# Kernel optimization log

Measured on AMD Instinct MI355X. Metric: run time of the kernel, lower is better.

Reference implementation:

```python
import jax, jax.numpy as jnp
import numpy as np

N_NODES = 100000
N_EDGES = 3200000
NFEAT, H1, H2, NCLASS = 512, 300, 200, 40


def setup_inputs() -> dict:
    key = jax.random.key(0)
    ks = jax.random.split(key, 8)
    x = jax.random.normal(ks[0], (N_NODES, NFEAT), dtype=jnp.float32)
    edge_index = jax.random.randint(ks[1], (2, N_EDGES), 0, N_NODES, dtype=jnp.int32)
    edge_weight = jax.random.uniform(ks[2], (N_EDGES,), dtype=jnp.float32)
    def glorot(k, fi, fo):
        s = 1.0 / np.sqrt(fi)
        return jax.random.uniform(k, (fi, fo), jnp.float32, -s, s)
    w1 = glorot(ks[3], NFEAT, H1)
    w2 = glorot(ks[4], H1, H2)
    w3 = glorot(ks[5], H2, NCLASS)
    return {
        'x': x, 'edge_index': edge_index, 'edge_weight': edge_weight,
        'w1': w1, 'b1': jnp.zeros((H1,), jnp.float32),
        'w2': w2, 'b2': jnp.zeros((H2,), jnp.float32),
        'w3': w3, 'b3': jnp.zeros((NCLASS,), jnp.float32),
    }


def _gcn_layer(h, edge_index, edge_weight, w, b):
    # support = h @ W ; out = A @ support + b  (A given as weighted edge list)
    support = h @ w                                   # [N, out]
    src, dst = edge_index[0], edge_index[1]
    msgs = support[src] * edge_weight[:, None]        # gather + scale, [E, out]
    agg = jax.ops.segment_sum(msgs, dst, num_segments=h.shape[0])
    return agg + b


def reference(x, edge_index, edge_weight, w1, b1, w2, b2, w3, b3):
    h1 = jax.nn.relu(_gcn_layer(x, edge_index, edge_weight, w1, b1))
    h2 = jax.nn.relu(_gcn_layer(h1, edge_index, edge_weight, w2, b2))
    logits = _gcn_layer(h2, edge_index, edge_weight, w3, b3)
    return jax.nn.softmax(logits, axis=1)
```

## Files before the change

### kernel.cpp

```cpp
#include <hip/hip_runtime.h>
#include <hip/hip_bf16.h>
#include <hip/hip_fp16.h>
#include <math.h>

#define NFEAT 512
#define H1 300
#define H2 200
#define NCLASS 40

typedef __attribute__((ext_vector_type(8))) _Float16 half8;
typedef __attribute__((ext_vector_type(4))) float f32x4;
typedef __attribute__((ext_vector_type(2))) unsigned int u32x2;

__device__ __forceinline__ void stage16(const void* gptr, void* ldsptr) {
    __builtin_amdgcn_global_load_lds(
        (const __attribute__((address_space(1))) unsigned int*)gptr,
        (__attribute__((address_space(3))) unsigned int*)ldsptr,
        16, 0, 0);
}

__device__ __forceinline__ unsigned short f2h(float f) {
    return __half_as_ushort(__float2half(f));
}
__device__ __forceinline__ float h2f(unsigned short u) {
    return __half2float(__ushort_as_half(u));
}
__device__ __forceinline__ float2 h2f2(unsigned int u) {
    __half2 h = *reinterpret_cast<__half2*>(&u);
    return __half22float2(h);
}
__device__ __forceinline__ unsigned pack2h(float a, float b) {
    return (unsigned)f2h(a) | ((unsigned)f2h(b) << 16);
}


__global__ __launch_bounds__(256) void count_dst_kernel(const int* __restrict__ dst,
                                                        int* __restrict__ counts, int E) {
    int i = blockIdx.x * blockDim.x + threadIdx.x;
    if (i < E) atomicAdd(&counts[dst[i]], 1);
}

__global__ __launch_bounds__(1024) void scan_kernel(const int* __restrict__ counts,
                                                    int* __restrict__ row_ptr,
                                                    int* __restrict__ nextp, int N) {
    __shared__ int sums[1024];
    const int tid = threadIdx.x;
    const int CH = (N + 1023) >> 10;
    const int b = tid * CH;
    const int e = min(b + CH, N);
    int s = 0;
    for (int i = b; i < e; i++) s += counts[i];
    sums[tid] = s;
    __syncthreads();
    #pragma unroll
    for (int off = 1; off < 1024; off <<= 1) {
        int t = (tid >= off) ? sums[tid - off] : 0;
        __syncthreads();
        sums[tid] += t;
        __syncthreads();
    }
    int run = (tid > 0) ? sums[tid - 1] : 0;
    for (int i = b; i < e; i++) {
        row_ptr[i] = run;
        nextp[i] = run;
        run += counts[i];
    }
    if (tid == 0) row_ptr[N] = sums[1023];
}

__global__ __launch_bounds__(256) void fill_csr_kernel(const int* __restrict__ src,
                                                       const int* __restrict__ dst,
                                                       const float* __restrict__ ew,
                                                       int* __restrict__ next,
                                                       int2* __restrict__ csr_sw, int E) {
    int i = blockIdx.x * blockDim.x + threadIdx.x;
    if (i < E) {
        int d = dst[i];
        int pos = atomicAdd(&next[d], 1);
        csr_sw[pos] = make_int2(src[i], __float_as_int(ew[i]));
    }
}


__global__ __launch_bounds__(256) void convert_x_kernel(const float* __restrict__ x,
                                                        unsigned short* __restrict__ X16,
                                                        int total8) {
    int stride = gridDim.x * 256;
    for (int i = blockIdx.x * 256 + threadIdx.x; i < total8; i += stride) {
        const float* p = x + (size_t)i * 8;
        float4 a = *(const float4*)p;
        float4 b = *(const float4*)(p + 4);
        half8 h;
        h[0] = (_Float16)a.x; h[1] = (_Float16)a.y;
        h[2] = (_Float16)a.z; h[3] = (_Float16)a.w;
        h[4] = (_Float16)b.x; h[5] = (_Float16)b.y;
        h[6] = (_Float16)b.z; h[7] = (_Float16)b.w;
        *(half8*)(X16 + (size_t)i * 8) = h;
    }
}


__global__ __launch_bounds__(256) void split_weights_kernel(
        const float* __restrict__ w1, const float* __restrict__ w2, const float* __restrict__ w3,
        unsigned short* __restrict__ W1H, unsigned short* __restrict__ W1L,
        unsigned short* __restrict__ W2H, unsigned short* __restrict__ W2L,
        unsigned short* __restrict__ W3H, unsigned short* __restrict__ W3L) {
    int i = blockIdx.x * 256 + threadIdx.x;
    const float* w; unsigned short *H, *L; int K, N, KP;
    if (i < 163840) {
        w = w1; H = W1H; L = W1L; K = 512; N = 300; KP = 512;
    } else if (i < 163840 + 81920) {
        i -= 163840; w = w2; H = W2H; L = W2L; K = 300; N = 200; KP = 320;
    } else {
        i -= 245760; w = w3; H = W3H; L = W3L; K = 200; N = 40; KP = 256;
    }
    int n = i / KP, k = i - n * KP;
    float a = (n < N && k < K) ? w[(size_t)k * N + n] : 0.f;
    unsigned short h = f2h(a);
    H[i] = h;
    L[i] = f2h(a - h2f(h));
}


template <int KPAD, int NT, bool AF32>
__global__ __launch_bounds__(256, 3) void gemm_f16_kernel(
        const void* __restrict__ A_,
        const unsigned short* __restrict__ Bhi, const unsigned short* __restrict__ Blo,
        unsigned short* __restrict__ C, int M, int NP, int MT) {
    __shared__ short Bs_hi[4096];
    __shared__ short Bs_lo[4096];

    const int id = blockIdx.x;
    const int g  = id / (8 * NT);
    const int r  = id % (8 * NT);
    const int nt = r >> 3;
    const int x  = r & 7;
    const int mt = g * 8 + x;
    if (mt >= MT) return;

    const int tid = threadIdx.x;
    const int wave = tid >> 6, lane = tid & 63;
    const int lm = lane & 15, quad = lane >> 4;
    const int bm = mt * 256, bn = nt * 64;

    f32x4 acc[4][4] = {};

    for (int k0 = 0; k0 < KPAD; k0 += 64) {
        #pragma unroll
        for (int i = 0; i < 2; i++) {
            int t = i * 256 + tid;
            int n = t >> 3;
            int c = (t & 7) ^ (n & 7);
            size_t goff = (size_t)(bn + n) * KPAD + (size_t)(k0 + c * 8);
            int lbase = (i * 256 + wave * 64) * 8;
            stage16(Bhi + goff, Bs_hi + lbase);
            stage16(Blo + goff, Bs_lo + lbase);
        }
        __syncthreads();

        #pragma unroll
        for (int h = 0; h < 2; h++) {
            const int cidx = h * 4 + quad;
            half8 a[4], bh[4], bl[4];
            #pragma unroll
            for (int i = 0; i < 4; i++) {
                int row = bm + wave * 64 + i * 16 + lm;
                row = row < M ? row : M - 1;
                size_t off = (size_t)row * KPAD + (size_t)(k0 + cidx * 8);
                if (AF32) {
                    const float* ap = (const float*)A_ + off;
                    float4 p = *(const float4*)ap;
                    float4 q = *(const float4*)(ap + 4);
                    half8 t8;
                    t8[0] = (_Float16)p.x; t8[1] = (_Float16)p.y;
                    t8[2] = (_Float16)p.z; t8[3] = (_Float16)p.w;
                    t8[4] = (_Float16)q.x; t8[5] = (_Float16)q.y;
                    t8[6] = (_Float16)q.z; t8[7] = (_Float16)q.w;
                    a[i] = t8;
                } else {
                    a[i] = *(const half8*)((const unsigned short*)A_ + off);
                }
            }
            #pragma unroll
            for (int j = 0; j < 4; j++) {
                int n = j * 16 + lm;
                int off = (n * 8 + (cidx ^ (n & 7))) * 8;
                bh[j] = *(const half8*)(Bs_hi + off);
                bl[j] = *(const half8*)(Bs_lo + off);
            }
            #pragma unroll
            for (int i = 0; i < 4; i++)
                #pragma unroll
                for (int j = 0; j < 4; j++) {
                    acc[i][j] = __builtin_amdgcn_mfma_f32_16x16x32_f16(a[i], bh[j], acc[i][j], 0, 0, 0);
                    acc[i][j] = __builtin_amdgcn_mfma_f32_16x16x32_f16(a[i], bl[j], acc[i][j], 0, 0, 0);
                }
        }
        __syncthreads();
    }

    #pragma unroll
    for (int i = 0; i < 4; i++) {
        #pragma unroll
        for (int j = 0; j < 4; j++) {
            #pragma unroll
            for (int r2 = 0; r2 < 4; r2++) {
                int row = bm + wave * 64 + i * 16 + quad * 4 + r2;
                int col = bn + j * 16 + lm;
                if (row < M)
                    C[(size_t)row * NP + col] = f2h(acc[i][j][r2]);
            }
        }
    }
}


template <int F, int NP>
__global__ __launch_bounds__(256) void spmm_relu_f16_kernel(
        const int* __restrict__ row_ptr, const int2* __restrict__ csr_sw,
        const unsigned short* __restrict__ support, const float* __restrict__ bias,
        unsigned short* __restrict__ outp, int N) {
    constexpr int F4 = F / 4;
    constexpr int NP4 = NP / 4;
    constexpr int NCH = (F4 + 63) / 64;
    constexpr int NCHW = (NP4 + 63) / 64;

    int row = blockIdx.x * 4 + (threadIdx.x >> 6);
    int lane = threadIdx.x & 63;
    if (row >= N) return;
    int beg = row_ptr[row], end = row_ptr[row + 1];

    float acc[NCHW][4] = {};

    int e = beg;
    int nb8 = (end - beg) >> 3;
    if (nb8 > 0) {
        int2 swbuf[8];
        #pragma unroll
        for (int q = 0; q < 8; q++) swbuf[q] = csr_sw[e + q];
        for (int b = 0; b < nb8; b++) {
            int s_[8]; float w_[8];
            #pragma unroll
            for (int q = 0; q < 8; q++) {
                s_[q] = __builtin_amdgcn_readfirstlane(swbuf[q].x);
                w_[q] = __uint_as_float((unsigned)__builtin_amdgcn_readfirstlane(swbuf[q].y));
            }
            u32x2 u[8][NCH];
            #pragma unroll
            for (int q = 0; q < 8; q++) {
                const unsigned short* sp = support + (size_t)s_[q] * NP;
                #pragma unroll
                for (int j = 0; j < NCH; j++) {
                    int f4 = j * 64 + lane;
                    if (f4 < F4) u[q][j] = *(const u32x2*)(sp + f4 * 4);
                }
            }
            int enext = e + 8;
            if (b + 1 < nb8) {
                #pragma unroll
                for (int q = 0; q < 8; q++) swbuf[q] = csr_sw[enext + q];
            }
            #pragma unroll
            for (int q = 0; q < 8; q++) {
                #pragma unroll
                for (int j = 0; j < NCH; j++) {
                    int f4 = j * 64 + lane;
                    if (f4 < F4) {
                        float2 a0 = h2f2(u[q][j].x), a1 = h2f2(u[q][j].y);
                        acc[j][0] += w_[q] * a0.x;
                        acc[j][1] += w_[q] * a0.y;
                        acc[j][2] += w_[q] * a1.x;
                        acc[j][3] += w_[q] * a1.y;
                    }
                }
            }
            e = enext;
        }
    }
    for (; e + 3 < end; e += 4) {
        int s_[4]; float w_[4];
        #pragma unroll
        for (int q = 0; q < 4; q++) {
            int2 sw = csr_sw[e + q];
            s_[q] = __builtin_amdgcn_readfirstlane(sw.x);
            w_[q] = __uint_as_float((unsigned)__builtin_amdgcn_readfirstlane(sw.y));
        }
        u32x2 u[4][NCH];
        #pragma unroll
        for (int q = 0; q < 4; q++) {
            const unsigned short* sp = support + (size_t)s_[q] * NP;
            #pragma unroll
            for (int j = 0; j < NCH; j++) {
                int f4 = j * 64 + lane;
                if (f4 < F4) u[q][j] = *(const u32x2*)(sp + f4 * 4);
            }
        }
        #pragma unroll
        for (int q = 0; q < 4; q++) {
            #pragma unroll
            for (int j = 0; j < NCH; j++) {
                int f4 = j * 64 + lane;
                if (f4 < F4) {
                    float2 a0 = h2f2(u[q][j].x), a1 = h2f2(u[q][j].y);
                    acc[j][0] += w_[q] * a0.x;
                    acc[j][1] += w_[q] * a0.y;
                    acc[j][2] += w_[q] * a1.x;
                    acc[j][3] += w_[q] * a1.y;
                }
            }
        }
    }
    for (; e < end; e++) {
        int2 sw = csr_sw[e];
        int ssrc = __builtin_amdgcn_readfirstlane(sw.x);
        float w0 = __uint_as_float((unsigned)__builtin_amdgcn_readfirstlane(sw.y));
        const unsigned short* sp = support + (size_t)ssrc * NP;
        #pragma unroll
        for (int j = 0; j < NCH; j++) {
            int f4 = j * 64 + lane;
            if (f4 < F4) {
                u32x2 u = *(const u32x2*)(sp + f4 * 4);
                float2 a0 = h2f2(u.x), a1 = h2f2(u.y);
                acc[j][0] += w0 * a0.x;
                acc[j][1] += w0 * a0.y;
                acc[j][2] += w0 * a1.x;
                acc[j][3] += w0 * a1.y;
            }
        }
    }

    #pragma unroll
    for (int j = 0; j < NCHW; j++) {
        int f4 = j * 64 + lane;
        if (f4 < NP4) {
            bool real = f4 < F4;
            float4 bb = real ? ((const float4*)bias)[f4] : make_float4(0, 0, 0, 0);
            float v0 = real ? fmaxf(acc[j][0] + bb.x, 0.f) : 0.f;
            float v1 = real ? fmaxf(acc[j][1] + bb.y, 0.f) : 0.f;
            float v2 = real ? fmaxf(acc[j][2] + bb.z, 0.f) : 0.f;
            float v3 = real ? fmaxf(acc[j][3] + bb.w, 0.f) : 0.f;
            u32x2 w;
            w.x = pack2h(v0, v1);
            w.y = pack2h(v2, v3);
            *(u32x2*)(outp + (size_t)row * NP + f4 * 4) = w;
        }
    }
}


__global__ __launch_bounds__(256) void spmm_softmax_kernel(
        const int* __restrict__ row_ptr, const int2* __restrict__ csr_sw,
        const unsigned short* __restrict__ support, const float* __restrict__ bias,
        float* __restrict__ out, int N) {
    int row = blockIdx.x * 4 + (threadIdx.x >> 6);
    int lane = threadIdx.x & 63;
    if (row >= N) return;
    int beg = row_ptr[row], end = row_ptr[row + 1];

    const int g = lane / 20;
    const int t = lane - g * 20;
    const bool lact = lane < 60;

    float a0 = 0.f, a1 = 0.f;
    for (int e = beg; e < end; e += 3) {
        int ei = e + g;
        bool v = lact && (ei < end);
        int2 sw = csr_sw[v ? ei : beg];
        float w = v ? __int_as_float(sw.y) : 0.f;
        unsigned u = *(const unsigned*)(support + (size_t)sw.x * 64 + t * 2);
        float2 aa = h2f2(u);
        a0 += w * aa.x;
        a1 += w * aa.y;
    }
    a0 += __shfl(a0, lane + 20) + __shfl(a0, lane + 40);
    a1 += __shfl(a1, lane + 20) + __shfl(a1, lane + 40);

    const bool act = lane < 20;
    float v0 = 0.f, v1 = 0.f, m = -INFINITY;
    if (act) {
        float2 bb = ((const float2*)bias)[t];
        v0 = a0 + bb.x;
        v1 = a1 + bb.y;
        m = fmaxf(v0, v1);
    }
    #pragma unroll
    for (int off = 16; off; off >>= 1) m = fmaxf(m, __shfl_xor(m, off));
    float e0 = 0.f, e1 = 0.f;
    if (act) { e0 = expf(v0 - m); e1 = expf(v1 - m); }
    float s = e0 + e1;
    #pragma unroll
    for (int off = 16; off; off >>= 1) s += __shfl_xor(s, off);
    if (act) {
        float inv = 1.f / s;
        *(float2*)(out + (size_t)row * NCLASS + t * 2) = make_float2(e0 * inv, e1 * inv);
    }
}


extern "C" void kernel_launch(void* const* d_in, const int* in_sizes, int n_in,
                              void* d_out, int out_size, void* d_ws, size_t ws_size,
                              hipStream_t stream) {
    const float* x   = (const float*)d_in[0];
    const int*   ei  = (const int*)d_in[1];
    const float* ew  = (const float*)d_in[2];
    const float* w1  = (const float*)d_in[3];
    const float* b1  = (const float*)d_in[4];
    const float* w2  = (const float*)d_in[5];
    const float* b2  = (const float*)d_in[6];
    const float* w3  = (const float*)d_in[7];
    const float* b3  = (const float*)d_in[8];
    float* out = (float*)d_out;

    const int N = in_sizes[0] / NFEAT;
    const int E = in_sizes[2];
    const int* src = ei;
    const int* dst = ei + E;

    const int KP1 = 512, NP1 = 320, NT1 = 5;
    const int KP2 = 320, NP2 = 256, NT2 = 4;
    const int KP3 = 256, NP3 = 64,  NT3 = 1;

    char* base = (char*)d_ws;
    unsigned short* X16 = (unsigned short*)(base);
    unsigned short* H1H = (unsigned short*)(base);
    unsigned short* H2H = (unsigned short*)(base);

    unsigned short* support = (unsigned short*)(base + 102400256);

    size_t wo = 102400256 + 64000256;
    auto walloc = [&](size_t bytes) { void* r = base + wo; wo += (bytes + 255) & ~(size_t)255; return r; };
    unsigned short* W1H = (unsigned short*)walloc((size_t)NP1 * KP1 * 2);
    unsigned short* W1L = (unsigned short*)walloc((size_t)NP1 * KP1 * 2);
    unsigned short* W2H = (unsigned short*)walloc((size_t)NP2 * KP2 * 2);
    unsigned short* W2L = (unsigned short*)walloc((size_t)NP2 * KP2 * 2);
    unsigned short* W3H = (unsigned short*)walloc((size_t)NP3 * KP3 * 2);
    unsigned short* W3L = (unsigned short*)walloc((size_t)NP3 * KP3 * 2);
    int*  counts  = (int*)walloc((size_t)N * 4);
    int*  row_ptr = (int*)walloc((size_t)(N + 1) * 4);
    int*  nextp   = (int*)walloc((size_t)N * 4);
    int2* csr_sw  = (int2*)walloc((size_t)E * 8);

    const int MT = (N + 255) / 256;
    const int G  = (MT + 7) / 8;
    const int wgs = (N + 3) / 4;

    hipMemsetAsync(counts, 0, (size_t)N * 4, stream);
    count_dst_kernel<<<(E + 255) / 256, 256, 0, stream>>>(dst, counts, E);
    scan_kernel<<<1, 1024, 0, stream>>>(counts, row_ptr, nextp, N);
    fill_csr_kernel<<<(E + 255) / 256, 256, 0, stream>>>(src, dst, ew, nextp, csr_sw, E);

    split_weights_kernel<<<1024, 256, 0, stream>>>(w1, w2, w3, W1H, W1L, W2H, W2L, W3H, W3L);
    convert_x_kernel<<<2048, 256, 0, stream>>>(x, X16, N * NFEAT / 8);

    gemm_f16_kernel<KP1, NT1, false><<<G * 8 * NT1, 256, 0, stream>>>(
        X16, W1H, W1L, support, N, NP1, MT);
    spmm_relu_f16_kernel<H1, NP1><<<wgs, 256, 0, stream>>>(row_ptr, csr_sw, support, b1, H1H, N);

    gemm_f16_kernel<KP2, NT2, false><<<G * 8 * NT2, 256, 0, stream>>>(
        H1H, W2H, W2L, support, N, NP2, MT);
    spmm_relu_f16_kernel<H2, NP2><<<wgs, 256, 0, stream>>>(row_ptr, csr_sw, support, b2, H2H, N);

    gemm_f16_kernel<KP3, NT3, false><<<G * 8 * NT3, 256, 0, stream>>>(
        H2H, W3H, W3L, support, N, NP3, MT);
    spmm_softmax_kernel<<<wgs, 256, 0, stream>>>(row_ptr, csr_sw, support, b3, out, N);
}
```

Before: 1.687 ms.

## Restructure SpMM kernels as persistent grid-stride waves with wide per-lane loads

The SpMM kernels become persistent: a fixed grid of 2048 blocks walks rows in grid-stride fashion instead of launching one wave per row. For H1, each lane now loads 8 halfs per neighbor in a single 16-byte load instead of two 8-byte chunks. Edge metadata is fetched with one vector load across lanes and broadcast with readlane, replacing the per-edge scalar loads and separate remainder loops. This cuts launch and instruction overhead, but a fixed grid can leave work unbalanced and partial batches still issue dummy loads with zero weight.

```diff
diff --git a/kernel.cpp b/kernel.cpp
--- a/kernel.cpp
+++ b/kernel.cpp
@@ -216,133 +216,86 @@
 
 
 template <int F, int NP>
-__global__ __launch_bounds__(256) void spmm_relu_f16_kernel(
+__global__ __launch_bounds__(256, 8) void spmm_relu_f16_kernel(
         const int* __restrict__ row_ptr, const int2* __restrict__ csr_sw,
         const unsigned short* __restrict__ support, const float* __restrict__ bias,
         unsigned short* __restrict__ outp, int N) {
-    constexpr int F4 = F / 4;
-    constexpr int NP4 = NP / 4;
-    constexpr int NCH = (F4 + 63) / 64;
-    constexpr int NCHW = (NP4 + 63) / 64;
-
-    int row = blockIdx.x * 4 + (threadIdx.x >> 6);
-    int lane = threadIdx.x & 63;
-    if (row >= N) return;
-    int beg = row_ptr[row], end = row_ptr[row + 1];
-
-    float acc[NCHW][4] = {};
-
-    int e = beg;
-    int nb8 = (end - beg) >> 3;
-    if (nb8 > 0) {
-        int2 swbuf[8];
-        #pragma unroll
-        for (int q = 0; q < 8; q++) swbuf[q] = csr_sw[e + q];
-        for (int b = 0; b < nb8; b++) {
+    constexpr bool WIDE = ((F + 3) / 4 > 64);
+    constexpr int LPE = WIDE ? (F + 7) / 8 : (F + 3) / 4;
+    constexpr int AK  = WIDE ? 8 : 4;
+
+    const int lane = threadIdx.x & 63;
+    const int nwaves = gridDim.x * 4;
+    const int lc = min(lane, LPE - 1);
+
+    for (int row = blockIdx.x * 4 + (threadIdx.x >> 6); row < N; row += nwaves) {
+        const int beg = row_ptr[row], end = row_ptr[row + 1];
+        float acc[AK];
+        #pragma unroll
+        for (int k = 0; k < AK; k++) acc[k] = 0.f;
+
+        int e = beg;
+        int2 swv;
+        if (e < end) swv = csr_sw[e + min(lane, min(end - e, 8) - 1)];
+        while (e < end) {
+            const int m = min(end - e, 8);
+            const int2 cur = swv;
             int s_[8]; float w_[8];
             #pragma unroll
             for (int q = 0; q < 8; q++) {
-                s_[q] = __builtin_amdgcn_readfirstlane(swbuf[q].x);
-                w_[q] = __uint_as_float((unsigned)__builtin_amdgcn_readfirstlane(swbuf[q].y));
-            }
-            u32x2 u[8][NCH];
+                int qq = min(q, m - 1);
+                s_[q] = __builtin_amdgcn_readlane(cur.x, qq);
+                float wv = __uint_as_float((unsigned)__builtin_amdgcn_readlane(cur.y, qq));
+                w_[q] = (q < m) ? wv : 0.f;
+            }
+            half8 u8[8]; u32x2 u4[8];
             #pragma unroll
             for (int q = 0; q < 8; q++) {
                 const unsigned short* sp = support + (size_t)s_[q] * NP;
+                if (WIDE) u8[q] = *(const half8*)(sp + lc * 8);
+                else      u4[q] = *(const u32x2*)(sp + lc * 4);
+            }
+            const int enext = e + m;
+            if (enext < end) swv = csr_sw[enext + min(lane, min(end - enext, 8) - 1)];
+            #pragma unroll
+            for (int q = 0; q < 8; q++) {
+                if (WIDE) {
+                    #pragma unroll
+                    for (int k = 0; k < 8; k++) acc[k] += w_[q] * (float)u8[q][k];
+                } else {
+                    float2 a0 = h2f2(u4[q].x), a1 = h2f2(u4[q].y);
+                    acc[0] += w_[q] * a0.x;
+                    acc[1] += w_[q] * a0.y;
+                    acc[2] += w_[q] * a1.x;
+                    acc[3] += w_[q] * a1.y;
+                }
+            }
+            e = enext;
+        }
+
+        if (WIDE) {
+            if (lane * 8 < NP) {
+                half8 o;
                 #pragma unroll
-                for (int j = 0; j < NCH; j++) {
-                    int f4 = j * 64 + lane;
-                    if (f4 < F4) u[q][j] = *(const u32x2*)(sp + f4 * 4);
+                for (int k = 0; k < 8; k++) {
+                    int f = lane * 8 + k;
+                    float v = 0.f;
+                    if (f < F && lane < LPE) v = fmaxf(acc[k] + bias[f], 0.f);
+                    o[k] = (_Float16)v;
                 }
-            }
-            int enext = e + 8;
-            if (b + 1 < nb8) {
-                #pragma unroll
-                for (int q = 0; q < 8; q++) swbuf[q] = csr_sw[enext + q];
-            }
-            #pragma unroll
-            for (int q = 0; q < 8; q++) {
-                #pragma unroll
-                for (int j = 0; j < NCH; j++) {
-                    int f4 = j * 64 + lane;
-                    if (f4 < F4) {
-                        float2 a0 = h2f2(u[q][j].x), a1 = h2f2(u[q][j].y);
-                        acc[j][0] += w_[q] * a0.x;
-                        acc[j][1] += w_[q] * a0.y;
-                        acc[j][2] += w_[q] * a1.x;
-                        acc[j][3] += w_[q] * a1.y;
-                    }
-                }
-            }
-            e = enext;
-        }
-    }
-    for (; e + 3 < end; e += 4) {
-        int s_[4]; float w_[4];
-        #pragma unroll
-        for (int q = 0; q < 4; q++) {
-            int2 sw = csr_sw[e + q];
-            s_[q] = __builtin_amdgcn_readfirstlane(sw.x);
-            w_[q] = __uint_as_float((unsigned)__builtin_amdgcn_readfirstlane(sw.y));
-        }
-        u32x2 u[4][NCH];
-        #pragma unroll
-        for (int q = 0; q < 4; q++) {
-            const unsigned short* sp = support + (size_t)s_[q] * NP;
-            #pragma unroll
-            for (int j = 0; j < NCH; j++) {
-                int f4 = j * 64 + lane;
-                if (f4 < F4) u[q][j] = *(const u32x2*)(sp + f4 * 4);
-            }
-        }
-        #pragma unroll
-        for (int q = 0; q < 4; q++) {
-            #pragma unroll
-            for (int j = 0; j < NCH; j++) {
-                int f4 = j * 64 + lane;
-                if (f4 < F4) {
-                    float2 a0 = h2f2(u[q][j].x), a1 = h2f2(u[q][j].y);
-                    acc[j][0] += w_[q] * a0.x;
-                    acc[j][1] += w_[q] * a0.y;
-                    acc[j][2] += w_[q] * a1.x;
-                    acc[j][3] += w_[q] * a1.y;
-                }
-            }
-        }
-    }
-    for (; e < end; e++) {
-        int2 sw = csr_sw[e];
-        int ssrc = __builtin_amdgcn_readfirstlane(sw.x);
-        float w0 = __uint_as_float((unsigned)__builtin_amdgcn_readfirstlane(sw.y));
-        const unsigned short* sp = support + (size_t)ssrc * NP;
-        #pragma unroll
-        for (int j = 0; j < NCH; j++) {
-            int f4 = j * 64 + lane;
-            if (f4 < F4) {
-                u32x2 u = *(const u32x2*)(sp + f4 * 4);
-                float2 a0 = h2f2(u.x), a1 = h2f2(u.y);
-                acc[j][0] += w0 * a0.x;
-                acc[j][1] += w0 * a0.y;
-                acc[j][2] += w0 * a1.x;
-                acc[j][3] += w0 * a1.y;
-            }
-        }
-    }
-
-    #pragma unroll
-    for (int j = 0; j < NCHW; j++) {
-        int f4 = j * 64 + lane;
-        if (f4 < NP4) {
-            bool real = f4 < F4;
-            float4 bb = real ? ((const float4*)bias)[f4] : make_float4(0, 0, 0, 0);
-            float v0 = real ? fmaxf(acc[j][0] + bb.x, 0.f) : 0.f;
-            float v1 = real ? fmaxf(acc[j][1] + bb.y, 0.f) : 0.f;
-            float v2 = real ? fmaxf(acc[j][2] + bb.z, 0.f) : 0.f;
-            float v3 = real ? fmaxf(acc[j][3] + bb.w, 0.f) : 0.f;
+                *(half8*)(outp + (size_t)row * NP + lane * 8) = o;
+            }
+        } else {
+            bool real = lane < LPE;
+            float4 bb = real ? ((const float4*)bias)[lane] : make_float4(0, 0, 0, 0);
+            float v0 = real ? fmaxf(acc[0] + bb.x, 0.f) : 0.f;
+            float v1 = real ? fmaxf(acc[1] + bb.y, 0.f) : 0.f;
+            float v2 = real ? fmaxf(acc[2] + bb.z, 0.f) : 0.f;
+            float v3 = real ? fmaxf(acc[3] + bb.w, 0.f) : 0.f;
             u32x2 w;
             w.x = pack2h(v0, v1);
             w.y = pack2h(v2, v3);
-            *(u32x2*)(outp + (size_t)row * NP + f4 * 4) = w;
+            *(u32x2*)(outp + (size_t)row * NP + lane * 4) = w;
         }
     }
 }
@@ -352,47 +305,49 @@
         const int* __restrict__ row_ptr, const int2* __restrict__ csr_sw,
         const unsigned short* __restrict__ support, const float* __restrict__ bias,
         float* __restrict__ out, int N) {
-    int row = blockIdx.x * 4 + (threadIdx.x >> 6);
-    int lane = threadIdx.x & 63;
-    if (row >= N) return;
-    int beg = row_ptr[row], end = row_ptr[row + 1];
+    const int lane = threadIdx.x & 63;
+    const int nwaves = gridDim.x * 4;
 
     const int g = lane / 20;
     const int t = lane - g * 20;
     const bool lact = lane < 60;
 
-    float a0 = 0.f, a1 = 0.f;
-    for (int e = beg; e < end; e += 3) {
-        int ei = e + g;
-        bool v = lact && (ei < end);
-        int2 sw = csr_sw[v ? ei : beg];
-        float w = v ? __int_as_float(sw.y) : 0.f;
-        unsigned u = *(const unsigned*)(support + (size_t)sw.x * 64 + t * 2);
-        float2 aa = h2f2(u);
-        a0 += w * aa.x;
-        a1 += w * aa.y;
-    }
-    a0 += __shfl(a0, lane + 20) + __shfl(a0, lane + 40);
-    a1 += __shfl(a1, lane + 20) + __shfl(a1, lane + 40);
-
-    const bool act = lane < 20;
-    float v0 = 0.f, v1 = 0.f, m = -INFINITY;
-    if (act) {
-        float2 bb = ((const float2*)bias)[t];
-        v0 = a0 + bb.x;
-        v1 = a1 + bb.y;
-        m = fmaxf(v0, v1);
-    }
-    #pragma unroll
-    for (int off = 16; off; off >>= 1) m = fmaxf(m, __shfl_xor(m, off));
-    float e0 = 0.f, e1 = 0.f;
-    if (act) { e0 = expf(v0 - m); e1 = expf(v1 - m); }
-    float s = e0 + e1;
-    #pragma unroll
-    for (int off = 16; off; off >>= 1) s += __shfl_xor(s, off);
-    if (act) {
-        float inv = 1.f / s;
-        *(float2*)(out + (size_t)row * NCLASS + t * 2) = make_float2(e0 * inv, e1 * inv);
+    for (int row = blockIdx.x * 4 + (threadIdx.x >> 6); row < N; row += nwaves) {
+        int beg = row_ptr[row], end = row_ptr[row + 1];
+
+        float a0 = 0.f, a1 = 0.f;
+        for (int e = beg; e < end; e += 3) {
+            int ei = e + g;
+            bool v = lact && (ei < end);
+            int2 sw = csr_sw[v ? ei : beg];
+            float w = v ? __int_as_float(sw.y) : 0.f;
+            unsigned u = *(const unsigned*)(support + (size_t)sw.x * 64 + t * 2);
+            float2 aa = h2f2(u);
+            a0 += w * aa.x;
+            a1 += w * aa.y;
+        }
+        a0 += __shfl(a0, lane + 20) + __shfl(a0, lane + 40);
+        a1 += __shfl(a1, lane + 20) + __shfl(a1, lane + 40);
+
+        const bool act = lane < 20;
+        float v0 = 0.f, v1 = 0.f, m = -INFINITY;
+        if (act) {
+            float2 bb = ((const float2*)bias)[t];
+            v0 = a0 + bb.x;
+            v1 = a1 + bb.y;
+            m = fmaxf(v0, v1);
+        }
+        #pragma unroll
+        for (int off = 16; off; off >>= 1) m = fmaxf(m, __shfl_xor(m, off));
+        float e0 = 0.f, e1 = 0.f;
+        if (act) { e0 = expf(v0 - m); e1 = expf(v1 - m); }
+        float s = e0 + e1;
+        #pragma unroll
+        for (int off = 16; off; off >>= 1) s += __shfl_xor(s, off);
+        if (act) {
+            float inv = 1.f / s;
+            *(float2*)(out + (size_t)row * NCLASS + t * 2) = make_float2(e0 * inv, e1 * inv);
+        }
     }
 }
 
@@ -442,7 +397,7 @@
 
     const int MT = (N + 255) / 256;
     const int G  = (MT + 7) / 8;
-    const int wgs = (N + 3) / 4;
+    const int SPMM_BLOCKS = 2048;
 
     hipMemsetAsync(counts, 0, (size_t)N * 4, stream);
     count_dst_kernel<<<(E + 255) / 256, 256, 0, stream>>>(dst, counts, E);
@@ -454,13 +409,13 @@
 
     gemm_f16_kernel<KP1, NT1, false><<<G * 8 * NT1, 256, 0, stream>>>(
         X16, W1H, W1L, support, N, NP1, MT);
-    spmm_relu_f16_kernel<H1, NP1><<<wgs, 256, 0, stream>>>(row_ptr, csr_sw, support, b1, H1H, N);
+    spmm_relu_f16_kernel<H1, NP1><<<SPMM_BLOCKS, 256, 0, stream>>>(row_ptr, csr_sw, support, b1, H1H, N);
 
     gemm_f16_kernel<KP2, NT2, false><<<G * 8 * NT2, 256, 0, stream>>>(
         H1H, W2H, W2L, support, N, NP2, MT);
-    spmm_relu_f16_kernel<H2, NP2><<<wgs, 256, 0, stream>>>(row_ptr, csr_sw, support, b2, H2H, N);
+    spmm_relu_f16_kernel<H2, NP2><<<SPMM_BLOCKS, 256, 0, stream>>>(row_ptr, csr_sw, support, b2, H2H, N);
 
     gemm_f16_kernel<KP3, NT3, false><<<G * 8 * NT3, 256, 0, stream>>>(
         H2H, W3H, W3L, support, N, NP3, MT);
-    spmm_softmax_kernel<<<wgs, 256, 0, stream>>>(row_ptr, csr_sw, support, b3, out, N);
-}
+    spmm_softmax_kernel<<<SPMM_BLOCKS, 256, 0, stream>>>(row_ptr, csr_sw, support, b3, out, N);
+}
```

After: 1.929 ms. 14.3% more time.

## Build CSR via two-pass counting sort for source locality; compact layer-2 support stride

Applied to the files above, without the earlier changes.

The CSR build becomes a two-pass stable counting sort. Edges are first bucketed by source, then by destination, so each destination row's neighbour list comes out ordered by source index. This should improve cache locality of the support gathers in the SpMM kernels. It also narrows the layer-2 support row stride from 256 to 200 halfs, which cuts gather bytes, at the price of less aligned rows and extra preprocessing passes with atomics.

```diff
diff --git a/kernel.cpp b/kernel.cpp
--- a/kernel.cpp
+++ b/kernel.cpp
@@ -34,10 +34,10 @@
 }
 
 
-__global__ __launch_bounds__(256) void count_dst_kernel(const int* __restrict__ dst,
+__global__ __launch_bounds__(256) void count_key_kernel(const int* __restrict__ key,
                                                         int* __restrict__ counts, int E) {
     int i = blockIdx.x * blockDim.x + threadIdx.x;
-    if (i < E) atomicAdd(&counts[dst[i]], 1);
+    if (i < E) atomicAdd(&counts[key[i]], 1);
 }
 
 __global__ __launch_bounds__(1024) void scan_kernel(const int* __restrict__ counts,
@@ -68,16 +68,30 @@
     if (tid == 0) row_ptr[N] = sums[1023];
 }
 
-__global__ __launch_bounds__(256) void fill_csr_kernel(const int* __restrict__ src,
-                                                       const int* __restrict__ dst,
-                                                       const float* __restrict__ ew,
-                                                       int* __restrict__ next,
-                                                       int2* __restrict__ csr_sw, int E) {
+__global__ __launch_bounds__(256) void scatter_src_kernel(const int* __restrict__ src,
+                                                          const int* __restrict__ dst,
+                                                          const float* __restrict__ ew,
+                                                          int* __restrict__ snext,
+                                                          int2* __restrict__ sw2,
+                                                          int* __restrict__ sdst, int E) {
     int i = blockIdx.x * blockDim.x + threadIdx.x;
     if (i < E) {
-        int d = dst[i];
+        int s = src[i];
+        int pos = atomicAdd(&snext[s], 1);
+        sw2[pos] = make_int2(s, __float_as_int(ew[i]));
+        sdst[pos] = dst[i];
+    }
+}
+
+__global__ __launch_bounds__(256) void fill_csr2_kernel(const int* __restrict__ sdst,
+                                                        const int2* __restrict__ sw2,
+                                                        int* __restrict__ next,
+                                                        int2* __restrict__ csr_sw, int E) {
+    int i = blockIdx.x * blockDim.x + threadIdx.x;
+    if (i < E) {
+        int d = sdst[i];
         int pos = atomicAdd(&next[d], 1);
-        csr_sw[pos] = make_int2(src[i], __float_as_int(ew[i]));
+        csr_sw[pos] = sw2[i];
     }
 }
 
@@ -207,7 +221,7 @@
             for (int r2 = 0; r2 < 4; r2++) {
                 int row = bm + wave * 64 + i * 16 + quad * 4 + r2;
                 int col = bn + j * 16 + lm;
-                if (row < M)
+                if (row < M && col < NP)
                     C[(size_t)row * NP + col] = f2h(acc[i][j][r2]);
             }
         }
@@ -215,13 +229,13 @@
 }
 
 
-template <int F, int NP>
+template <int F, int NPS, int NPO>
 __global__ __launch_bounds__(256) void spmm_relu_f16_kernel(
         const int* __restrict__ row_ptr, const int2* __restrict__ csr_sw,
         const unsigned short* __restrict__ support, const float* __restrict__ bias,
         unsigned short* __restrict__ outp, int N) {
     constexpr int F4 = F / 4;
-    constexpr int NP4 = NP / 4;
+    constexpr int NP4 = NPO / 4;
     constexpr int NCH = (F4 + 63) / 64;
     constexpr int NCHW = (NP4 + 63) / 64;
 
@@ -248,7 +262,7 @@
             u32x2 u[8][NCH];
             #pragma unroll
             for (int q = 0; q < 8; q++) {
-                const unsigned short* sp = support + (size_t)s_[q] * NP;
+                const unsigned short* sp = support + (size_t)s_[q] * NPS;
                 #pragma unroll
                 for (int j = 0; j < NCH; j++) {
                     int f4 = j * 64 + lane;
@@ -288,7 +302,7 @@
         u32x2 u[4][NCH];
         #pragma unroll
         for (int q = 0; q < 4; q++) {
-            const unsigned short* sp = support + (size_t)s_[q] * NP;
+            const unsigned short* sp = support + (size_t)s_[q] * NPS;
             #pragma unroll
             for (int j = 0; j < NCH; j++) {
                 int f4 = j * 64 + lane;
@@ -314,7 +328,7 @@
         int2 sw = csr_sw[e];
         int ssrc = __builtin_amdgcn_readfirstlane(sw.x);
         float w0 = __uint_as_float((unsigned)__builtin_amdgcn_readfirstlane(sw.y));
-        const unsigned short* sp = support + (size_t)ssrc * NP;
+        const unsigned short* sp = support + (size_t)ssrc * NPS;
         #pragma unroll
         for (int j = 0; j < NCH; j++) {
             int f4 = j * 64 + lane;
@@ -342,7 +356,7 @@
             u32x2 w;
             w.x = pack2h(v0, v1);
             w.y = pack2h(v2, v3);
-            *(u32x2*)(outp + (size_t)row * NP + f4 * 4) = w;
+            *(u32x2*)(outp + (size_t)row * NPO + f4 * 4) = w;
         }
     }
 }
@@ -417,10 +431,12 @@
     const int* dst = ei + E;
 
     const int KP1 = 512, NP1 = 320, NT1 = 5;
-    const int KP2 = 320, NP2 = 256, NT2 = 4;
+    const int KP2 = 320, NP2 = 200, NT2 = 4;
     const int KP3 = 256, NP3 = 64,  NT3 = 1;
 
     char* base = (char*)d_ws;
+    int2* sw2  = (int2*)base;
+    int*  sdst = (int*)(base + (size_t)E * 8);
     unsigned short* X16 = (unsigned short*)(base);
     unsigned short* H1H = (unsigned short*)(base);
     unsigned short* H2H = (unsigned short*)(base);
@@ -429,12 +445,12 @@
 
     size_t wo = 102400256 + 64000256;
     auto walloc = [&](size_t bytes) { void* r = base + wo; wo += (bytes + 255) & ~(size_t)255; return r; };
-    unsigned short* W1H = (unsigned short*)walloc((size_t)NP1 * KP1 * 2);
-    unsigned short* W1L = (unsigned short*)walloc((size_t)NP1 * KP1 * 2);
-    unsigned short* W2H = (unsigned short*)walloc((size_t)NP2 * KP2 * 2);
-    unsigned short* W2L = (unsigned short*)walloc((size_t)NP2 * KP2 * 2);
-    unsigned short* W3H = (unsigned short*)walloc((size_t)NP3 * KP3 * 2);
-    unsigned short* W3L = (unsigned short*)walloc((size_t)NP3 * KP3 * 2);
+    unsigned short* W1H = (unsigned short*)walloc((size_t)320 * 512 * 2);
+    unsigned short* W1L = (unsigned short*)walloc((size_t)320 * 512 * 2);
+    unsigned short* W2H = (unsigned short*)walloc((size_t)256 * 320 * 2);
+    unsigned short* W2L = (unsigned short*)walloc((size_t)256 * 320 * 2);
+    unsigned short* W3H = (unsigned short*)walloc((size_t)64 * 256 * 2);
+    unsigned short* W3L = (unsigned short*)walloc((size_t)64 * 256 * 2);
     int*  counts  = (int*)walloc((size_t)N * 4);
     int*  row_ptr = (int*)walloc((size_t)(N + 1) * 4);
     int*  nextp   = (int*)walloc((size_t)N * 4);
@@ -444,21 +460,27 @@
     const int G  = (MT + 7) / 8;
     const int wgs = (N + 3) / 4;
 
+    const int EB = (E + 255) / 256;
+
     hipMemsetAsync(counts, 0, (size_t)N * 4, stream);
-    count_dst_kernel<<<(E + 255) / 256, 256, 0, stream>>>(dst, counts, E);
+    count_key_kernel<<<EB, 256, 0, stream>>>(src, counts, E);
     scan_kernel<<<1, 1024, 0, stream>>>(counts, row_ptr, nextp, N);
-    fill_csr_kernel<<<(E + 255) / 256, 256, 0, stream>>>(src, dst, ew, nextp, csr_sw, E);
+    scatter_src_kernel<<<EB, 256, 0, stream>>>(src, dst, ew, nextp, sw2, sdst, E);
+    hipMemsetAsync(counts, 0, (size_t)N * 4, stream);
+    count_key_kernel<<<EB, 256, 0, stream>>>(sdst, counts, E);
+    scan_kernel<<<1, 1024, 0, stream>>>(counts, row_ptr, nextp, N);
+    fill_csr2_kernel<<<EB, 256, 0, stream>>>(sdst, sw2, nextp, csr_sw, E);
 
     split_weights_kernel<<<1024, 256, 0, stream>>>(w1, w2, w3, W1H, W1L, W2H, W2L, W3H, W3L);
     convert_x_kernel<<<2048, 256, 0, stream>>>(x, X16, N * NFEAT / 8);
 
     gemm_f16_kernel<KP1, NT1, false><<<G * 8 * NT1, 256, 0, stream>>>(
         X16, W1H, W1L, support, N, NP1, MT);
-    spmm_relu_f16_kernel<H1, NP1><<<wgs, 256, 0, stream>>>(row_ptr, csr_sw, support, b1, H1H, N);
+    spmm_relu_f16_kernel<H1, 320, 320><<<wgs, 256, 0, stream>>>(row_ptr, csr_sw, support, b1, H1H, N);
 
     gemm_f16_kernel<KP2, NT2, false><<<G * 8 * NT2, 256, 0, stream>>>(
         H1H, W2H, W2L, support, N, NP2, MT);
-    spmm_relu_f16_kernel<H2, NP2><<<wgs, 256, 0, stream>>>(row_ptr, csr_sw, support, b2, H2H, N);
+    spmm_relu_f16_kernel<H2, 200, 256><<<wgs, 256, 0, stream>>>(row_ptr, csr_sw, support, b2, H2H, N);
 
     gemm_f16_kernel<KP3, NT3, false><<<G * 8 * NT3, 256, 0, stream>>>(
         H2H, W3H, W3L, support, N, NP3, MT);
```

Result: slower. 2.242 ms (+32.9%).
